# Performance work log

Measured on AMD Instinct MI355X. Metric: run time of the kernel, lower is better.

## Reference

```python
import jax, jax.numpy as jnp
import numpy as np

T, V, L, N, D = 4, 2, 3, 4000, 256
TEMP = 0.5


def setup_inputs() -> dict:
    key = jax.random.key(0)
    ks = jax.random.split(key, 9)
    E = jax.random.normal(ks[0], (T, V, L, N, D), dtype=jnp.float32)
    s = 1.0 / np.sqrt(D)
    W1 = jax.random.uniform(ks[1], (D, D), jnp.float32, -s, s)
    b1 = jax.random.uniform(ks[2], (D,), jnp.float32, -s, s)
    W2 = jax.random.uniform(ks[3], (D, D), jnp.float32, -s, s)
    b2 = jax.random.uniform(ks[4], (D,), jnp.float32, -s, s)
    idx_prio = jax.random.randint(ks[5], (2, V, L, 100), 0, N, dtype=jnp.int32)
    idx_rest = jax.random.randint(ks[6], (2, V, L, 20), 0, N, dtype=jnp.int32)
    neg_idx_prio = jax.random.randint(ks[7], (2, V, L, 3, 50), 0, N, dtype=jnp.int32)
    neg_idx_rest = jax.random.randint(ks[8], (2, V, L, 3, 10), 0, N, dtype=jnp.int32)
    return {
        "node_embeddings": E, "W1": W1, "b1": b1, "W2": W2, "b2": b2,
        "idx_prio": idx_prio, "idx_rest": idx_rest,
        "neg_idx_prio": neg_idx_prio, "neg_idx_rest": neg_idx_rest,
        "num_views": 2, "num_layers": 3,
    }


def _proj_norm(x, W1, b1, W2, b2):
    # nn.Linear -> ReLU -> nn.Linear, then F.normalize(p=2, dim=-1)
    h = jax.nn.relu(x @ W1.T + b1)
    z = h @ W2.T + b2
    return z / jnp.maximum(jnp.linalg.norm(z, axis=-1, keepdims=True), 1e-12)


def _type_loss(P, t, idx, nidx):
    # P: [T,V,L,N,D] projected+normalized; idx: [V,L,S] anchor node ids;
    # nidx: [V,L,3,K] cross-type negative node ids (one row per other type).
    vi = jnp.arange(V)[:, None, None]
    li = jnp.arange(L)[None, :, None]
    z = P[t][vi, li, idx]                                  # [V,L,S,D] anchors
    # positives: same node index across every other (view, layer) combo
    Pj = P[t][:, :, idx, :]                                # [X,Y,V,L,S,D]
    sims_pos = jnp.einsum('vlsd,xyvlsd->vlsxy', z, Pj) / TEMP
    same_vl = (jnp.eye(V, dtype=bool)[:, None, :, None]
               & jnp.eye(L, dtype=bool)[None, :, None, :])  # [V,L,X,Y]
    pos = jnp.where(same_vl[:, :, None, :, :], 0.0,
                    jnp.exp(sims_pos)).sum((-2, -1))        # [V,L,S]
    # within-type negatives: the other sampled anchors at the same (v,l)
    S = idx.shape[-1]
    sims_in = jnp.einsum('vlsd,vltd->vlst', z, z) / TEMP
    neg_in = jnp.where(jnp.eye(S, dtype=bool), 0.0,
                       jnp.exp(sims_in)).sum(-1)            # [V,L,S]
    # cross-type negatives: K sampled nodes from each other type at (v,l)
    others = jnp.array([o for o in range(T) if o != t])
    Po = P[others]                                          # [3,V,L,N,D]
    nidx2 = jnp.moveaxis(nidx, 2, 0)                        # [3,V,L,K]
    Pneg = jnp.take_along_axis(Po, nidx2[..., None], axis=3)  # [3,V,L,K,D]
    sims_c = jnp.einsum('vlsd,ovlkd->vlsok', z, Pneg) / TEMP
    neg = neg_in + jnp.exp(sims_c).sum((-2, -1))            # [V,L,S]
    loss = -jnp.log(pos / (pos + neg))
    return loss.sum(), loss.size


def reference(node_embeddings, W1, b1, W2, b2, idx_prio, idx_rest,
              neg_idx_prio, neg_idx_rest, num_views, num_layers):
    P = _proj_norm(node_embeddings, W1, b1, W2, b2)  # [T,V,L,N,D]
    total = jnp.float32(0.0)
    count = 0
    for t in range(T):  # small fixed loop over node types
        if t < 2:
            ls, c = _type_loss(P, t, idx_prio[t], neg_idx_prio[t])
        else:
            ls, c = _type_loss(P, t, idx_rest[t - 2], neg_idx_rest[t - 2])
        total = total + ls
        count += c
    return total / count
```

## Files before the change

kernel.cpp:

```cpp
#include <hip/hip_runtime.h>
#include <math.h>

#define DD 256
#define NV 2
#define NL 3
#define NNODE 4000
#define NROWS_B 8640
#define NROWS 10800
#define NANCH 1440
#define ACC_OFF (10800L * 128)
#define CNT_IDX (ACC_OFF + 2 * NANCH)
#define WP_OFF (ACC_OFF + 2 * NANCH + 4)
#define XPAD 260
#define NBLK_SIM 96

typedef __attribute__((ext_vector_type(8))) short short8;
typedef __attribute__((ext_vector_type(4))) short short4v;
typedef __attribute__((ext_vector_type(4))) float f32x4;

__device__ __forceinline__ unsigned short f2bf(float f) {
  unsigned u = __float_as_uint(f);
  u += 0x7fff + ((u >> 16) & 1);
  return (unsigned short)(u >> 16);
}

__device__ __forceinline__ int tb_B(int t) { return (t < 2) ? t * 3600 : 7200 + (t - 2) * 720; }
__device__ __forceinline__ int tb_C(int t) { return (t < 2) ? t * 900 : 1800 + (t - 2) * 180; }
__device__ __forceinline__ int anch_base(int t, int vl) {
  return ((t < 2) ? t * 600 : 1200 + (t - 2) * 120) + vl * ((t < 2) ? 100 : 20);
}

__device__ __forceinline__ long row_src(int u, const int* __restrict__ ip,
                                        const int* __restrict__ ir,
                                        const int* __restrict__ npg,
                                        const int* __restrict__ nrg) {
  int t, x, y, node;
  if (u < NROWS_B) {
    int S, u2;
    if (u < 7200) { t = u / 3600; u2 = u - t * 3600; S = 100; }
    else { int w = u - 7200; t = 2 + w / 720; u2 = w % 720; S = 20; }
    int s = u2 % S; int t1 = u2 / S;
    int l = t1 % NL; int t2 = t1 / NL;
    int v = t2 % NV; int xy = t2 / NV;
    x = xy / NL; y = xy % NL;
    if (t < 2) node = ip[((t * NV + v) * NL + l) * 100 + s];
    else       node = ir[(((t - 2) * NV + v) * NL + l) * 20 + s];
  } else {
    int w = u - NROWS_B;
    int K, u2;
    if (w < 1800) { t = w / 900; u2 = w % 900; K = 50; }
    else { int w2 = w - 1800; t = 2 + w2 / 180; u2 = w2 % 180; K = 10; }
    int k = u2 % K; int t1 = u2 / K;
    int l = t1 % NL; int t2 = t1 / NL;
    int v = t2 % NV; int o = t2 / NV;
    if (t < 2) node = npg[(((t * NV + v) * NL + l) * 3 + o) * 50 + k];
    else       node = nrg[((((t - 2) * NV + v) * NL + l) * 3 + o) * 10 + k];
    int ot = (o < t) ? o : o + 1;
    t = ot; x = v; y = l;
  }
  return ((((long)t * NV + x) * NL + y) * NNODE + node) * DD;
}

__global__ __launch_bounds__(256) void k_prep(const float* __restrict__ W1,
                                              const float* __restrict__ W2,
                                              float* __restrict__ ws) {
  int tid = blockIdx.x * 256 + threadIdx.x;
  if (tid < 2 * NANCH + 4) ws[ACC_OFF + tid] = 0.0f;
  int st = tid >> 13, rem = tid & 8191;
  int cg = rem >> 9, kstep = (rem >> 6) & 7, lane = rem & 63;
  const float* W = st ? W2 : W1;
  int col = cg * 16 + (lane & 15);
  int k0 = kstep * 32 + (lane >> 4) * 8;
  unsigned short v[8] __attribute__((aligned(16)));
#pragma unroll
  for (int j = 0; j < 8; ++j) v[j] = f2bf(W[col * DD + k0 + j]);
  unsigned short* wp = (unsigned short*)(ws + WP_OFF);
  *(uint4*)(wp + (long)tid * 8) = *(const uint4*)v;
}

__global__ __launch_bounds__(256) void k_proj(const float* __restrict__ E,
                                              const float* __restrict__ b1,
                                              const float* __restrict__ b2,
                                              const int* __restrict__ ip,
                                              const int* __restrict__ ir,
                                              const int* __restrict__ npg,
                                              const int* __restrict__ nrg,
                                              float* __restrict__ ws) {
  __shared__ unsigned short Xs[32][XPAD];
  __shared__ unsigned short Hs[32][XPAD];
  __shared__ float ssbuf[2][32];
  const int tid = threadIdx.x;
  const int u0 = blockIdx.x * 32;
  const int wv = tid >> 6, l64 = tid & 63;
  const int quad = l64 >> 4, l15 = l64 & 15;
  const int rhalf = wv & 1, chalf = wv >> 1;
  const int rb = rhalf * 16, cb = chalf * 128;
  const unsigned short* wp = (const unsigned short*)(ws + WP_OFF);
  unsigned short* zb = (unsigned short*)ws;

  for (int i = 0; i < 8; ++i) {
    int r = wv * 8 + i;
    int u = u0 + r;
    float4 val = make_float4(0.f, 0.f, 0.f, 0.f);
    if (u < NROWS) {
      long src = row_src(u, ip, ir, npg, nrg);
      val = *(const float4*)(E + src + l64 * 4);
    }
    unsigned short h[4] __attribute__((aligned(8)));
    h[0] = f2bf(val.x); h[1] = f2bf(val.y); h[2] = f2bf(val.z); h[3] = f2bf(val.w);
    *(uint2*)(&Xs[r][l64 * 4]) = *(const uint2*)h;
  }

  f32x4 acc[8];
#pragma unroll
  for (int cg = 0; cg < 8; ++cg) {
    float bv = b1[cb + cg * 16 + l15];
    acc[cg] = (f32x4){bv, bv, bv, bv};
  }
  __syncthreads();
#pragma unroll
  for (int ks = 0; ks < 8; ++ks) {
    const unsigned short* ap = &Xs[rb + l15][ks * 32 + quad * 8];
    short4v alo = *(const short4v*)(ap);
    short4v ahi = *(const short4v*)(ap + 4);
    short8 a = __builtin_shufflevector(alo, ahi, 0, 1, 2, 3, 4, 5, 6, 7);
#pragma unroll
    for (int cg = 0; cg < 8; ++cg) {
      short8 b = *(const short8*)(wp + ((long)(((chalf * 8 + cg) * 8 + ks) * 64 + l64)) * 8);
      acc[cg] = __builtin_amdgcn_mfma_f32_16x16x32_bf16(a, b, acc[cg], 0, 0, 0);
    }
  }
#pragma unroll
  for (int cg = 0; cg < 8; ++cg) {
    int col = cb + cg * 16 + l15;
#pragma unroll
    for (int reg = 0; reg < 4; ++reg) {
      int row = rb + quad * 4 + reg;
      Hs[row][col] = f2bf(fmaxf(acc[cg][reg], 0.0f));
    }
  }
#pragma unroll
  for (int cg = 0; cg < 8; ++cg) {
    float bv = b2[cb + cg * 16 + l15];
    acc[cg] = (f32x4){bv, bv, bv, bv};
  }
  __syncthreads();
#pragma unroll
  for (int ks = 0; ks < 8; ++ks) {
    const unsigned short* ap = &Hs[rb + l15][ks * 32 + quad * 8];
    short4v alo = *(const short4v*)(ap);
    short4v ahi = *(const short4v*)(ap + 4);
    short8 a = __builtin_shufflevector(alo, ahi, 0, 1, 2, 3, 4, 5, 6, 7);
#pragma unroll
    for (int cg = 0; cg < 8; ++cg) {
      short8 b = *(const short8*)(wp + ((long)((16 + chalf * 8 + cg) * 8 + ks) * 64 + l64) * 8);
      acc[cg] = __builtin_amdgcn_mfma_f32_16x16x32_bf16(a, b, acc[cg], 0, 0, 0);
    }
  }
  float ss[4];
#pragma unroll
  for (int reg = 0; reg < 4; ++reg) {
    float s = 0.f;
#pragma unroll
    for (int cg = 0; cg < 8; ++cg) s = fmaf(acc[cg][reg], acc[cg][reg], s);
    ss[reg] = s;
  }
#pragma unroll
  for (int m = 1; m < 16; m <<= 1) {
#pragma unroll
    for (int reg = 0; reg < 4; ++reg) ss[reg] += __shfl_xor(ss[reg], m, 64);
  }
  if (l15 == 0) {
#pragma unroll
    for (int reg = 0; reg < 4; ++reg) ssbuf[chalf][rb + quad * 4 + reg] = ss[reg];
  }
  __syncthreads();
#pragma unroll
  for (int reg = 0; reg < 4; ++reg) {
    int row = rb + quad * 4 + reg;
    int u = u0 + row;
    if (u < NROWS) {
      float tot = ssbuf[0][row] + ssbuf[1][row];
      float sc = 1.0f / fmaxf(sqrtf(tot), 1e-12f);
#pragma unroll
      for (int cg = 0; cg < 8; ++cg)
        zb[(long)u * DD + cb + cg * 16 + l15] = f2bf(acc[cg][reg] * sc);
    }
  }
}

__global__ __launch_bounds__(256) void k_sim(float* __restrict__ ws,
                                             float* __restrict__ out) {
  __shared__ float negL[112];
  __shared__ float red[256];
  __shared__ int lastFlag;
  const unsigned short* zb = (const unsigned short*)ws;
  float* posG = ws + ACC_OFF;
  float* negG = ws + ACC_OFF + NANCH;
  int* cnt = (int*)(ws + CNT_IDX);

  const int b = blockIdx.x;
  int t, vl, c;
  if (b < 72) { t = b / 36; int r = b % 36; vl = r / 6; c = r % 6; }
  else { int q = b - 72; t = 2 + q / 12; int r2 = q % 12; vl = r2 / 2; c = r2 % 2; }
  const int v = vl / NL, l = vl % NL;
  const int S = (t < 2) ? 100 : 20, K = (t < 2) ? 50 : 10;
  const int Ptot = 6 * S + 3 * K;
  const int q0 = c * 128;
  const int rem = Ptot - q0;
  const int NT = ((rem < 128 ? rem : 128) + 15) / 16;
  const int MT = (S + 15) / 16;
  const int tid = threadIdx.x;
  const int wv = tid >> 6, l64 = tid & 63;
  const int quad = l64 >> 4, l15 = l64 & 15;
  const int ab = anch_base(t, vl);
  const int rowZbase = tb_B(t) + ((vl * NV + v) * NL + l) * S;

  for (int mt = wv; mt < MT; mt += 4) {
    int am = mt * 16 + l15;
    int amc = (am < S) ? am : (S - 1);
    const unsigned short* abase = zb + (long)(rowZbase + amc) * DD + quad * 8;
    short8 afr[8];
#pragma unroll
    for (int ks = 0; ks < 8; ++ks) afr[ks] = *(const short8*)(abase + ks * 32);
    float negAcc[4] = {0.f, 0.f, 0.f, 0.f};
    for (int nt = 0; nt < NT; ++nt) {
      int qg = q0 + nt * 16 + l15;
      bool vq = (qg < Ptot);
      int qc = vq ? qg : 0;
      int rowb, xy = -1, j = -1;
      if (qc < 6 * S) {
        xy = qc / S; j = qc - xy * S;
        rowb = tb_B(t) + ((xy * NV + v) * NL + l) * S + j;
      } else {
        int q2 = qc - 6 * S; int o = q2 / K, k2 = q2 - o * K;
        rowb = NROWS_B + tb_C(t) + ((o * NV + v) * NL + l) * K + k2;
      }
      const unsigned short* bbase = zb + (long)rowb * DD + quad * 8;
      f32x4 acc = {0.f, 0.f, 0.f, 0.f};
#pragma unroll
      for (int ks = 0; ks < 8; ++ks) {
        short8 bfr = *(const short8*)(bbase + ks * 32);
        acc = __builtin_amdgcn_mfma_f32_16x16x32_bf16(afr[ks], bfr, acc, 0, 0, 0);
      }
#pragma unroll
      for (int r = 0; r < 4; ++r) {
        int a = mt * 16 + quad * 4 + r;
        if (!vq || a >= S) continue;
        float e = expf(2.0f * acc[r]);
        if (xy >= 0) {
          if (xy == vl) { if (j != a) negAcc[r] += e; }
          else if (j == a) atomicAdd(&posG[ab + a], e);
        } else {
          negAcc[r] += e;
        }
      }
    }
#pragma unroll
    for (int m = 1; m < 16; m <<= 1) {
#pragma unroll
      for (int r = 0; r < 4; ++r) negAcc[r] += __shfl_xor(negAcc[r], m, 64);
    }
    if (l15 == 0) {
#pragma unroll
      for (int r = 0; r < 4; ++r) negL[mt * 16 + quad * 4 + r] = negAcc[r];
    }
  }
  __syncthreads();
  for (int a = tid; a < S; a += 256) atomicAdd(&negG[ab + a], negL[a]);
  __threadfence();
  __syncthreads();
  if (tid == 0) {
    int old = atomicAdd(cnt, 1);
    lastFlag = (old == NBLK_SIM - 1) ? 1 : 0;
  }
  __syncthreads();
  if (lastFlag) {
    float sum = 0.f;
    for (int i = tid; i < NANCH; i += 256) {
      float p = atomicAdd(&posG[i], 0.0f);
      float n = atomicAdd(&negG[i], 0.0f);
      sum += -logf(p / (p + n));
    }
    red[tid] = sum;
    __syncthreads();
    for (int s = 128; s > 0; s >>= 1) {
      if (tid < s) red[tid] += red[tid + s];
      __syncthreads();
    }
    if (tid == 0) out[0] = red[0] / (float)NANCH;
  }
}

extern "C" void kernel_launch(void* const* d_in, const int* in_sizes, int n_in,
                              void* d_out, int out_size, void* d_ws, size_t ws_size,
                              hipStream_t stream) {
  const float* E  = (const float*)d_in[0];
  const float* W1 = (const float*)d_in[1];
  const float* b1 = (const float*)d_in[2];
  const float* W2 = (const float*)d_in[3];
  const float* b2 = (const float*)d_in[4];
  const int* ip  = (const int*)d_in[5];
  const int* ir  = (const int*)d_in[6];
  const int* npg = (const int*)d_in[7];
  const int* nrg = (const int*)d_in[8];
  float* ws = (float*)d_ws;
  float* out = (float*)d_out;

  hipLaunchKernelGGL(k_prep, dim3(64), dim3(256), 0, stream, W1, W2, ws);
  hipLaunchKernelGGL(k_proj, dim3((NROWS + 31) / 32), dim3(256), 0, stream,
                     E, b1, b2, ip, ir, npg, nrg, ws);
  hipLaunchKernelGGL(k_sim, dim3(NBLK_SIM), dim3(256), 0, stream, ws, out);
}
```

Baseline: 214.9 us.

## Split projection into 16-row blocks and sim into per-wave fine-grained tasks

The projection kernel now processes 16 rows per block, with each wave owning 64 output columns instead of a 2x2 row/column split, which doubles the grid to 675 blocks and drops the bounds checks. The similarity kernel is rewritten so that each wave handles one 16-anchor by 32-candidate tile task, giving 534 blocks instead of 96, and negatives are atomically added per wave. This targets under-occupancy of the GPU in both kernels. In exchange it adds more global atomics and more redundant anchor fragment loads.

```diff
diff --git a/kernel.cpp b/kernel.cpp
--- a/kernel.cpp
+++ b/kernel.cpp
@@ -12,7 +12,8 @@
 #define CNT_IDX (ACC_OFF + 2 * NANCH)
 #define WP_OFF (ACC_OFF + 2 * NANCH + 4)
 #define XPAD 260
-#define NBLK_SIM 96
+#define NTASK 2136
+#define NBLK_SIM (NTASK / 4)
 
 typedef __attribute__((ext_vector_type(8))) short short8;
 typedef __attribute__((ext_vector_type(4))) short short4v;
@@ -86,74 +87,71 @@
                                               const int* __restrict__ npg,
                                               const int* __restrict__ nrg,
                                               float* __restrict__ ws) {
-  __shared__ unsigned short Xs[32][XPAD];
-  __shared__ unsigned short Hs[32][XPAD];
-  __shared__ float ssbuf[2][32];
+  __shared__ unsigned short Xs[16][XPAD];
+  __shared__ unsigned short Hs[16][XPAD];
+  __shared__ float ssbuf[4][16];
   const int tid = threadIdx.x;
-  const int u0 = blockIdx.x * 32;
+  const int u0 = blockIdx.x * 16;
   const int wv = tid >> 6, l64 = tid & 63;
   const int quad = l64 >> 4, l15 = l64 & 15;
-  const int rhalf = wv & 1, chalf = wv >> 1;
-  const int rb = rhalf * 16, cb = chalf * 128;
+  const int cb = wv * 64;
   const unsigned short* wp = (const unsigned short*)(ws + WP_OFF);
   unsigned short* zb = (unsigned short*)ws;
 
-  for (int i = 0; i < 8; ++i) {
-    int r = wv * 8 + i;
+  for (int i = 0; i < 4; ++i) {
+    int r = wv * 4 + i;
     int u = u0 + r;
-    float4 val = make_float4(0.f, 0.f, 0.f, 0.f);
-    if (u < NROWS) {
-      long src = row_src(u, ip, ir, npg, nrg);
-      val = *(const float4*)(E + src + l64 * 4);
-    }
+    long src = row_src(u, ip, ir, npg, nrg);
+    float4 val = *(const float4*)(E + src + l64 * 4);
     unsigned short h[4] __attribute__((aligned(8)));
     h[0] = f2bf(val.x); h[1] = f2bf(val.y); h[2] = f2bf(val.z); h[3] = f2bf(val.w);
     *(uint2*)(&Xs[r][l64 * 4]) = *(const uint2*)h;
   }
 
-  f32x4 acc[8];
-#pragma unroll
-  for (int cg = 0; cg < 8; ++cg) {
+  f32x4 acc[4];
+#pragma unroll
+  for (int cg = 0; cg < 4; ++cg) {
     float bv = b1[cb + cg * 16 + l15];
     acc[cg] = (f32x4){bv, bv, bv, bv};
   }
   __syncthreads();
 #pragma unroll
   for (int ks = 0; ks < 8; ++ks) {
-    const unsigned short* ap = &Xs[rb + l15][ks * 32 + quad * 8];
+    const unsigned short* ap = &Xs[l15][ks * 32 + quad * 8];
     short4v alo = *(const short4v*)(ap);
     short4v ahi = *(const short4v*)(ap + 4);
     short8 a = __builtin_shufflevector(alo, ahi, 0, 1, 2, 3, 4, 5, 6, 7);
 #pragma unroll
-    for (int cg = 0; cg < 8; ++cg) {
-      short8 b = *(const short8*)(wp + ((long)(((chalf * 8 + cg) * 8 + ks) * 64 + l64)) * 8);
+    for (int cg = 0; cg < 4; ++cg) {
+      short8 b = *(const short8*)(wp + ((long)(((wv * 4 + cg) * 8 + ks) * 64 + l64)) * 8);
       acc[cg] = __builtin_amdgcn_mfma_f32_16x16x32_bf16(a, b, acc[cg], 0, 0, 0);
     }
   }
-#pragma unroll
-  for (int cg = 0; cg < 8; ++cg) {
+  __syncthreads();
+#pragma unroll
+  for (int cg = 0; cg < 4; ++cg) {
     int col = cb + cg * 16 + l15;
 #pragma unroll
     for (int reg = 0; reg < 4; ++reg) {
-      int row = rb + quad * 4 + reg;
+      int row = quad * 4 + reg;
       Hs[row][col] = f2bf(fmaxf(acc[cg][reg], 0.0f));
     }
   }
 #pragma unroll
-  for (int cg = 0; cg < 8; ++cg) {
+  for (int cg = 0; cg < 4; ++cg) {
     float bv = b2[cb + cg * 16 + l15];
     acc[cg] = (f32x4){bv, bv, bv, bv};
   }
   __syncthreads();
 #pragma unroll
   for (int ks = 0; ks < 8; ++ks) {
-    const unsigned short* ap = &Hs[rb + l15][ks * 32 + quad * 8];
+    const unsigned short* ap = &Hs[l15][ks * 32 + quad * 8];
     short4v alo = *(const short4v*)(ap);
     short4v ahi = *(const short4v*)(ap + 4);
     short8 a = __builtin_shufflevector(alo, ahi, 0, 1, 2, 3, 4, 5, 6, 7);
 #pragma unroll
-    for (int cg = 0; cg < 8; ++cg) {
-      short8 b = *(const short8*)(wp + ((long)((16 + chalf * 8 + cg) * 8 + ks) * 64 + l64) * 8);
+    for (int cg = 0; cg < 4; ++cg) {
+      short8 b = *(const short8*)(wp + ((long)((16 + wv * 4 + cg) * 8 + ks) * 64 + l64) * 8);
       acc[cg] = __builtin_amdgcn_mfma_f32_16x16x32_bf16(a, b, acc[cg], 0, 0, 0);
     }
   }
@@ -162,7 +160,7 @@
   for (int reg = 0; reg < 4; ++reg) {
     float s = 0.f;
 #pragma unroll
-    for (int cg = 0; cg < 8; ++cg) s = fmaf(acc[cg][reg], acc[cg][reg], s);
+    for (int cg = 0; cg < 4; ++cg) s = fmaf(acc[cg][reg], acc[cg][reg], s);
     ss[reg] = s;
   }
 #pragma unroll
@@ -172,26 +170,23 @@
   }
   if (l15 == 0) {
 #pragma unroll
-    for (int reg = 0; reg < 4; ++reg) ssbuf[chalf][rb + quad * 4 + reg] = ss[reg];
+    for (int reg = 0; reg < 4; ++reg) ssbuf[wv][quad * 4 + reg] = ss[reg];
   }
   __syncthreads();
 #pragma unroll
   for (int reg = 0; reg < 4; ++reg) {
-    int row = rb + quad * 4 + reg;
+    int row = quad * 4 + reg;
     int u = u0 + row;
-    if (u < NROWS) {
-      float tot = ssbuf[0][row] + ssbuf[1][row];
-      float sc = 1.0f / fmaxf(sqrtf(tot), 1e-12f);
-#pragma unroll
-      for (int cg = 0; cg < 8; ++cg)
-        zb[(long)u * DD + cb + cg * 16 + l15] = f2bf(acc[cg][reg] * sc);
-    }
+    float tot = ssbuf[0][row] + ssbuf[1][row] + ssbuf[2][row] + ssbuf[3][row];
+    float sc = 1.0f / fmaxf(sqrtf(tot), 1e-12f);
+#pragma unroll
+    for (int cg = 0; cg < 4; ++cg)
+      zb[(long)u * DD + cb + cg * 16 + l15] = f2bf(acc[cg][reg] * sc);
   }
 }
 
 __global__ __launch_bounds__(256) void k_sim(float* __restrict__ ws,
                                              float* __restrict__ out) {
-  __shared__ float negL[112];
   __shared__ float red[256];
   __shared__ int lastFlag;
   const unsigned short* zb = (const unsigned short*)ws;
@@ -199,75 +194,75 @@
   float* negG = ws + ACC_OFF + NANCH;
   int* cnt = (int*)(ws + CNT_IDX);
 
-  const int b = blockIdx.x;
-  int t, vl, c;
-  if (b < 72) { t = b / 36; int r = b % 36; vl = r / 6; c = r % 6; }
-  else { int q = b - 72; t = 2 + q / 12; int r2 = q % 12; vl = r2 / 2; c = r2 % 2; }
+  const int tid = threadIdx.x;
+  const int wv = tid >> 6, l64 = tid & 63;
+  const int quad = l64 >> 4, l15 = l64 & 15;
+  const int task = blockIdx.x * 4 + wv;
+
+  int t, vl, mt, c;
+  if (task < 2016) { t = task / 1008; int r = task % 1008;
+                     vl = r / 168; int r2 = r % 168; mt = r2 / 24; c = r2 % 24; }
+  else { int q = task - 2016; t = 2 + q / 60; int r2 = q % 60;
+         vl = r2 / 10; int r3 = r2 % 10; mt = r3 / 5; c = r3 % 5; }
   const int v = vl / NL, l = vl % NL;
   const int S = (t < 2) ? 100 : 20, K = (t < 2) ? 50 : 10;
   const int Ptot = 6 * S + 3 * K;
-  const int q0 = c * 128;
-  const int rem = Ptot - q0;
-  const int NT = ((rem < 128 ? rem : 128) + 15) / 16;
-  const int MT = (S + 15) / 16;
-  const int tid = threadIdx.x;
-  const int wv = tid >> 6, l64 = tid & 63;
-  const int quad = l64 >> 4, l15 = l64 & 15;
   const int ab = anch_base(t, vl);
   const int rowZbase = tb_B(t) + ((vl * NV + v) * NL + l) * S;
 
-  for (int mt = wv; mt < MT; mt += 4) {
-    int am = mt * 16 + l15;
-    int amc = (am < S) ? am : (S - 1);
-    const unsigned short* abase = zb + (long)(rowZbase + amc) * DD + quad * 8;
-    short8 afr[8];
-#pragma unroll
-    for (int ks = 0; ks < 8; ++ks) afr[ks] = *(const short8*)(abase + ks * 32);
-    float negAcc[4] = {0.f, 0.f, 0.f, 0.f};
-    for (int nt = 0; nt < NT; ++nt) {
-      int qg = q0 + nt * 16 + l15;
-      bool vq = (qg < Ptot);
-      int qc = vq ? qg : 0;
-      int rowb, xy = -1, j = -1;
-      if (qc < 6 * S) {
-        xy = qc / S; j = qc - xy * S;
-        rowb = tb_B(t) + ((xy * NV + v) * NL + l) * S + j;
+  int am = mt * 16 + l15;
+  int amc = (am < S) ? am : (S - 1);
+  const unsigned short* abase = zb + (long)(rowZbase + amc) * DD + quad * 8;
+  short8 afr[8];
+#pragma unroll
+  for (int ks = 0; ks < 8; ++ks) afr[ks] = *(const short8*)(abase + ks * 32);
+
+  float negAcc[4] = {0.f, 0.f, 0.f, 0.f};
+#pragma unroll
+  for (int nt = 0; nt < 2; ++nt) {
+    int qg = c * 32 + nt * 16 + l15;
+    bool vq = (qg < Ptot);
+    int qc = vq ? qg : 0;
+    int rowb, xy = -1, j = -1;
+    if (qc < 6 * S) {
+      xy = qc / S; j = qc - xy * S;
+      rowb = tb_B(t) + ((xy * NV + v) * NL + l) * S + j;
+    } else {
+      int q2 = qc - 6 * S; int o = q2 / K, k2 = q2 - o * K;
+      rowb = NROWS_B + tb_C(t) + ((o * NV + v) * NL + l) * K + k2;
+    }
+    const unsigned short* bbase = zb + (long)rowb * DD + quad * 8;
+    f32x4 acc = {0.f, 0.f, 0.f, 0.f};
+#pragma unroll
+    for (int ks = 0; ks < 8; ++ks) {
+      short8 bfr = *(const short8*)(bbase + ks * 32);
+      acc = __builtin_amdgcn_mfma_f32_16x16x32_bf16(afr[ks], bfr, acc, 0, 0, 0);
+    }
+#pragma unroll
+    for (int r = 0; r < 4; ++r) {
+      int a = mt * 16 + quad * 4 + r;
+      if (!vq || a >= S) continue;
+      float e = expf(2.0f * acc[r]);
+      if (xy >= 0) {
+        if (xy == vl) { if (j != a) negAcc[r] += e; }
+        else if (j == a) atomicAdd(&posG[ab + a], e);
       } else {
-        int q2 = qc - 6 * S; int o = q2 / K, k2 = q2 - o * K;
-        rowb = NROWS_B + tb_C(t) + ((o * NV + v) * NL + l) * K + k2;
+        negAcc[r] += e;
       }
-      const unsigned short* bbase = zb + (long)rowb * DD + quad * 8;
-      f32x4 acc = {0.f, 0.f, 0.f, 0.f};
-#pragma unroll
-      for (int ks = 0; ks < 8; ++ks) {
-        short8 bfr = *(const short8*)(bbase + ks * 32);
-        acc = __builtin_amdgcn_mfma_f32_16x16x32_bf16(afr[ks], bfr, acc, 0, 0, 0);
-      }
-#pragma unroll
-      for (int r = 0; r < 4; ++r) {
-        int a = mt * 16 + quad * 4 + r;
-        if (!vq || a >= S) continue;
-        float e = expf(2.0f * acc[r]);
-        if (xy >= 0) {
-          if (xy == vl) { if (j != a) negAcc[r] += e; }
-          else if (j == a) atomicAdd(&posG[ab + a], e);
-        } else {
-          negAcc[r] += e;
-        }
-      }
-    }
-#pragma unroll
-    for (int m = 1; m < 16; m <<= 1) {
-#pragma unroll
-      for (int r = 0; r < 4; ++r) negAcc[r] += __shfl_xor(negAcc[r], m, 64);
-    }
-    if (l15 == 0) {
-#pragma unroll
-      for (int r = 0; r < 4; ++r) negL[mt * 16 + quad * 4 + r] = negAcc[r];
-    }
-  }
-  __syncthreads();
-  for (int a = tid; a < S; a += 256) atomicAdd(&negG[ab + a], negL[a]);
+    }
+  }
+#pragma unroll
+  for (int m = 1; m < 16; m <<= 1) {
+#pragma unroll
+    for (int r = 0; r < 4; ++r) negAcc[r] += __shfl_xor(negAcc[r], m, 64);
+  }
+  if (l15 == 0) {
+#pragma unroll
+    for (int r = 0; r < 4; ++r) {
+      int a = mt * 16 + quad * 4 + r;
+      if (a < S) atomicAdd(&negG[ab + a], negAcc[r]);
+    }
+  }
   __threadfence();
   __syncthreads();
   if (tid == 0) {
@@ -308,7 +303,7 @@
   float* out = (float*)d_out;
 
   hipLaunchKernelGGL(k_prep, dim3(64), dim3(256), 0, stream, W1, W2, ws);
-  hipLaunchKernelGGL(k_proj, dim3((NROWS + 31) / 32), dim3(256), 0, stream,
+  hipLaunchKernelGGL(k_proj, dim3(NROWS / 16), dim3(256), 0, stream,
                      E, b1, b2, ip, ir, npg, nrg, ws);
   hipLaunchKernelGGL(k_sim, dim3(NBLK_SIM), dim3(256), 0, stream, ws, out);
 }
```

New measurement: 203.2 us. -5.4%, faster.
